# Optimization experiments

Measured on AMD Instinct MI355X. Metric: run time of the kernel, lower is better.

The kernel has to match this reference:

```python
import jax, jax.numpy as jnp
import numpy as np

H1, H2 = 32, 16


def _gru_layer(x, W_ih, W_hh, b_ih, b_hh, H):
    # x: [B, T, I]; W_ih: [3H, I]; W_hh: [3H, H]; biases: [3H]
    # PyTorch gate order: r, z, n
    B = x.shape[0]
    xW = jnp.einsum('bti,gi->btg', x, W_ih) + b_ih  # [B, T, 3H]

    def step(h, xw_t):
        gh = h @ W_hh.T + b_hh                      # [B, 3H]
        r = jax.nn.sigmoid(xw_t[:, :H] + gh[:, :H])
        z = jax.nn.sigmoid(xw_t[:, H:2 * H] + gh[:, H:2 * H])
        n = jnp.tanh(xw_t[:, 2 * H:] + r * gh[:, 2 * H:])
        h_new = (1.0 - z) * n + z * h
        return h_new, h_new

    h0 = jnp.zeros((B, H), dtype=x.dtype)
    _, ys = jax.lax.scan(step, h0, jnp.swapaxes(xW, 0, 1))  # ys: [T, B, H]
    return jnp.swapaxes(ys, 0, 1)


def setup_inputs() -> dict:
    key = jax.random.key(0)
    ks = jax.random.split(key, 11)
    B, I, T, O = 4096, 8, 512, 1

    def u(k, shape, fan):
        s = 1.0 / np.sqrt(fan)
        return jax.random.uniform(k, shape, jnp.float32, -s, s)

    return {
        'input_seq': jax.random.normal(ks[0], (B, I, T), jnp.float32),
        'W_ih1': u(ks[1], (3 * H1, I), H1),
        'W_hh1': u(ks[2], (3 * H1, H1), H1),
        'b_ih1': u(ks[3], (3 * H1,), H1),
        'b_hh1': u(ks[4], (3 * H1,), H1),
        'W_ih2': u(ks[5], (3 * H2, H1), H2),
        'W_hh2': u(ks[6], (3 * H2, H2), H2),
        'b_ih2': u(ks[7], (3 * H2,), H2),
        'b_hh2': u(ks[8], (3 * H2,), H2),
        'W_lin': u(ks[9], (O, H2), H2),
        'b_lin': u(ks[10], (O,), H2),
    }


def reference(input_seq, W_ih1, W_hh1, b_ih1, b_hh1,
              W_ih2, W_hh2, b_ih2, b_hh2, W_lin, b_lin):
    x = jnp.transpose(input_seq, (0, 2, 1))          # [B, T, I]
    h1 = _gru_layer(x, W_ih1, W_hh1, b_ih1, b_hh1, H1)   # [B, T, 32]
    h2 = _gru_layer(h1, W_ih2, W_hh2, b_ih2, b_hh2, H2)  # [B, T, 16]
    out = h2[:, -1, :] @ W_lin.T + b_lin             # [B, O]
    return jnp.squeeze(out)                          # [B] when O == 1
```

## Files before the change

### kernel.cpp

```cpp
#include <hip/hip_runtime.h>

typedef __attribute__((ext_vector_type(4))) float    f32x4;
typedef __attribute__((ext_vector_type(4))) unsigned u32x4;

#define LOG2E 1.44269504088896340736f
__device__ __forceinline__ float fexp2(float x){ return __builtin_amdgcn_exp2f(x); }
__device__ __forceinline__ float frcp (float x){ return __builtin_amdgcn_rcpf(x); }
__device__ __forceinline__ float sigf (float x){ return frcp(1.0f + fexp2(-LOG2E*x)); }
__device__ __forceinline__ float tanh_(float x){ return 1.0f - 2.0f*frcp(1.0f + fexp2(2.0f*LOG2E*x)); }

__device__ __forceinline__ unsigned rne_bf16(float f){
    unsigned u = __builtin_bit_cast(unsigned, f);
    return (u + 0x7fffu + ((u >> 16) & 1u)) >> 16;
}
__device__ __forceinline__ u32x4 packdup4(const float* p){
    u32x4 r;
    #pragma unroll
    for (int q = 0; q < 4; ++q) {
        unsigned w = rne_bf16(p[q]);
        r[q] = w | (w << 16);
    }
    return r;
}
__device__ __forceinline__ unsigned packsplit(float h){
    unsigned hu = __builtin_bit_cast(unsigned, h);
    unsigned hm = hu & 0xffff0000u;
    float rem = h - __builtin_bit_cast(float, hm);
    unsigned ru = __builtin_bit_cast(unsigned, rem);
    return (hm >> 16) | (ru & 0xffff0000u);
}

#define MFMA_INIT(d, a, b, c) asm("v_mfma_f32_16x16x32_bf16 %0, %1, %2, %3" : "=&v"(d) : "v"(a), "v"(b), "v"(c))
#define MFMA_ACC(acc, a, b)   asm("v_mfma_f32_16x16x32_bf16 %0, %1, %2, %0" : "+v"(acc) : "v"(a), "v"(b))

__global__ __launch_bounds__(192)
void gru2_mfma(const float* __restrict__ x_g,
               const float* __restrict__ Wih1, const float* __restrict__ Whh1,
               const float* __restrict__ bih1, const float* __restrict__ bhh1,
               const float* __restrict__ Wih2, const float* __restrict__ Whh2,
               const float* __restrict__ bih2, const float* __restrict__ bhh2,
               const float* __restrict__ Wlin, const float* __restrict__ blin,
               float* __restrict__ out)
{
    const int tid = threadIdx.x;
    const int wid = tid / 64;
    const int l   = tid & 63;
    const int sl  = l & 15;
    const int g   = l >> 4;
    const int b0  = blockIdx.x * 16;

    __shared__ unsigned xpk[32][16][12];
    __shared__ unsigned h1b[2][16][36];
    __shared__ unsigned h2b[2][16][20];
    __shared__ unsigned zl[4];

    {
        unsigned* p1 = &h1b[0][0][0];
        for (int k = tid; k < 2*16*36; k += 192) p1[k] = 0u;
        unsigned* p2 = &h2b[0][0][0];
        for (int k = tid; k < 2*16*20; k += 192) p2[k] = 0u;
        if (tid < 4) zl[tid] = 0u;
    }

    u32x4 fR0, fR1, fR2, fZ0, fZ1, fZ2, fX0, fA, fB;
    f32x4 cbR, cbZ, cbX, cbH;
    const u32x4 zero4 = {0u, 0u, 0u, 0u};

    if (wid < 2) {
        const int Ub = wid * 16;
        const int gr = Ub + sl, gz = 32 + Ub + sl, gn = 64 + Ub + sl;
        fR0 = (g < 2) ? packdup4(Wih1 + gr*8  + 4*g) : zero4;
        fR1 = packdup4(Whh1 + gr*32 + 4*g);
        fR2 = packdup4(Whh1 + gr*32 + 16 + 4*g);
        fZ0 = (g < 2) ? packdup4(Wih1 + gz*8  + 4*g) : zero4;
        fZ1 = packdup4(Whh1 + gz*32 + 4*g);
        fZ2 = packdup4(Whh1 + gz*32 + 16 + 4*g);
        fX0 = (g < 2) ? packdup4(Wih1 + gn*8  + 4*g) : zero4;
        fA  = packdup4(Whh1 + gn*32 + 4*g);
        fB  = packdup4(Whh1 + gn*32 + 16 + 4*g);
        #pragma unroll
        for (int e = 0; e < 4; ++e) {
            const int u = Ub + 4*g + e;
            cbR[e] = bih1[u]      + bhh1[u];
            cbZ[e] = bih1[32+u]   + bhh1[32+u];
            cbX[e] = bih1[64+u];
            cbH[e] = bhh1[64+u];
        }
    } else {
        fR0 = packdup4(Wih2 + sl*32 + 4*g);
        fR1 = packdup4(Wih2 + sl*32 + 16 + 4*g);
        fR2 = packdup4(Whh2 + sl*16 + 4*g);
        fZ0 = packdup4(Wih2 + (16+sl)*32 + 4*g);
        fZ1 = packdup4(Wih2 + (16+sl)*32 + 16 + 4*g);
        fZ2 = packdup4(Whh2 + (16+sl)*16 + 4*g);
        fX0 = packdup4(Wih2 + (32+sl)*32 + 4*g);
        fA  = packdup4(Wih2 + (32+sl)*32 + 16 + 4*g);
        fB  = packdup4(Whh2 + (32+sl)*16 + 4*g);
        #pragma unroll
        for (int e = 0; e < 4; ++e) {
            const int u = 4*g + e;
            cbR[e] = bih2[u]    + bhh2[u];
            cbZ[e] = bih2[16+u] + bhh2[16+u];
            cbX[e] = bih2[32+u];
            cbH[e] = bhh2[32+u];
        }
    }

    float hv[4] = {0.f, 0.f, 0.f, 0.f};

    #pragma unroll 1
    for (int i = 0; i <= 512; ++i) {
        if ((i & 31) == 0 && i < 512) {
            if (tid < 128) {
                const int s  = tid >> 3;
                const int ii = tid & 7;
                const float* xg = x_g + ((size_t)(b0 + s))*4096 + ii*512 + i;
                #pragma unroll
                for (int w4 = 0; w4 < 8; ++w4) {
                    const f32x4 v = *(const f32x4*)(xg + 4*w4);
                    #pragma unroll
                    for (int e = 0; e < 4; ++e)
                        xpk[w4*4 + e][s][ii] = packsplit(v[e]);
                }
            }
            __syncthreads();
        }

        const int pr = (i + 1) & 1;

        if (wid < 2 && i < 512) {
            const int tt = i & 31;
            const u32x4 bT0 = (g < 2) ? *(const u32x4*)&xpk[tt][sl][4*g]
                                      : *(const u32x4*)&zl[0];
            const u32x4 bT1 = *(const u32x4*)&h1b[pr][sl][4*g];
            const u32x4 bT2 = *(const u32x4*)&h1b[pr][sl][16 + 4*g];
            f32x4 cr, cz, cx, cn;
            MFMA_INIT(cr, fR0, bT0, cbR); MFMA_ACC(cr, fR1, bT1); MFMA_ACC(cr, fR2, bT2);
            MFMA_INIT(cz, fZ0, bT0, cbZ); MFMA_ACC(cz, fZ1, bT1); MFMA_ACC(cz, fZ2, bT2);
            MFMA_INIT(cx, fX0, bT0, cbX);
            MFMA_INIT(cn, fA,  bT1, cbH); MFMA_ACC(cn, fB, bT2);
            unsigned wr0, wr1, wr2, wr3;
            {
                float r, z, n, h;
                r = sigf(cr[0]); z = sigf(cz[0]); n = tanh_(fmaf(r, cn[0], cx[0]));
                h = n + z*(hv[0]-n); hv[0] = h; wr0 = packsplit(h);
                r = sigf(cr[1]); z = sigf(cz[1]); n = tanh_(fmaf(r, cn[1], cx[1]));
                h = n + z*(hv[1]-n); hv[1] = h; wr1 = packsplit(h);
                r = sigf(cr[2]); z = sigf(cz[2]); n = tanh_(fmaf(r, cn[2], cx[2]));
                h = n + z*(hv[2]-n); hv[2] = h; wr2 = packsplit(h);
                r = sigf(cr[3]); z = sigf(cz[3]); n = tanh_(fmaf(r, cn[3], cx[3]));
                h = n + z*(hv[3]-n); hv[3] = h; wr3 = packsplit(h);
            }
            u32x4 wv = {wr0, wr1, wr2, wr3};
            *(u32x4*)&h1b[i & 1][sl][(wid ? 16 : 0) + 4*g] = wv;
        }

        if (wid == 2 && i > 0) {
            const u32x4 bU0 = *(const u32x4*)&h1b[pr][sl][4*g];
            const u32x4 bU1 = *(const u32x4*)&h1b[pr][sl][16 + 4*g];
            const u32x4 bU2 = *(const u32x4*)&h2b[i & 1][sl][4*g];
            f32x4 cr, cz, cx, cn;
            MFMA_INIT(cr, fR0, bU0, cbR); MFMA_ACC(cr, fR1, bU1); MFMA_ACC(cr, fR2, bU2);
            MFMA_INIT(cz, fZ0, bU0, cbZ); MFMA_ACC(cz, fZ1, bU1); MFMA_ACC(cz, fZ2, bU2);
            MFMA_INIT(cx, fX0, bU0, cbX); MFMA_ACC(cx, fA, bU1);
            MFMA_INIT(cn, fB,  bU2, cbH);
            unsigned wr0, wr1, wr2, wr3;
            {
                float r, z, n, h;
                r = sigf(cr[0]); z = sigf(cz[0]); n = tanh_(fmaf(r, cn[0], cx[0]));
                h = n + z*(hv[0]-n); hv[0] = h; wr0 = packsplit(h);
                r = sigf(cr[1]); z = sigf(cz[1]); n = tanh_(fmaf(r, cn[1], cx[1]));
                h = n + z*(hv[1]-n); hv[1] = h; wr1 = packsplit(h);
                r = sigf(cr[2]); z = sigf(cz[2]); n = tanh_(fmaf(r, cn[2], cx[2]));
                h = n + z*(hv[2]-n); hv[2] = h; wr2 = packsplit(h);
                r = sigf(cr[3]); z = sigf(cz[3]); n = tanh_(fmaf(r, cn[3], cx[3]));
                h = n + z*(hv[3]-n); hv[3] = h; wr3 = packsplit(h);
            }
            u32x4 wv = {wr0, wr1, wr2, wr3};
            *(u32x4*)&h2b[(i + 1) & 1][sl][4*g] = wv;
        }

        __syncthreads();
    }

    if (wid == 2) {
        float acc = 0.0f;
        acc = fmaf(Wlin[4*g+0], hv[0], acc);
        acc = fmaf(Wlin[4*g+1], hv[1], acc);
        acc = fmaf(Wlin[4*g+2], hv[2], acc);
        acc = fmaf(Wlin[4*g+3], hv[3], acc);
        acc += __shfl_xor(acc, 16, 64);
        acc += __shfl_xor(acc, 32, 64);
        if (g == 0) out[b0 + sl] = acc + blin[0];
    }
}

extern "C" void kernel_launch(void* const* d_in, const int* in_sizes, int n_in,
                              void* d_out, int out_size, void* d_ws, size_t ws_size,
                              hipStream_t stream) {
    const float* x    = (const float*)d_in[0];
    const float* Wih1 = (const float*)d_in[1];
    const float* Whh1 = (const float*)d_in[2];
    const float* bih1 = (const float*)d_in[3];
    const float* bhh1 = (const float*)d_in[4];
    const float* Wih2 = (const float*)d_in[5];
    const float* Whh2 = (const float*)d_in[6];
    const float* bih2 = (const float*)d_in[7];
    const float* bhh2 = (const float*)d_in[8];
    const float* Wlin = (const float*)d_in[9];
    const float* blin = (const float*)d_in[10];
    float* out = (float*)d_out;

    dim3 grid(256), block(192);
    hipLaunchKernelGGL(gru2_mfma, grid, block, 0, stream,
                       x, Wih1, Whh1, bih1, bhh1, Wih2, Whh2, bih2, bhh2,
                       Wlin, blin, out);
}
```

Baseline: 260.2 us.

## Add bf16 low-part weight MFMAs and keep own hidden state in registers

```diff
diff --git a/kernel.cpp b/kernel.cpp
--- a/kernel.cpp
+++ b/kernel.cpp
@@ -2,12 +2,18 @@
 
 typedef __attribute__((ext_vector_type(4))) float    f32x4;
 typedef __attribute__((ext_vector_type(4))) unsigned u32x4;
+typedef __attribute__((ext_vector_type(8))) short    s16x8;
 
 #define LOG2E 1.44269504088896340736f
 __device__ __forceinline__ float fexp2(float x){ return __builtin_amdgcn_exp2f(x); }
 __device__ __forceinline__ float frcp (float x){ return __builtin_amdgcn_rcpf(x); }
 __device__ __forceinline__ float sigf (float x){ return frcp(1.0f + fexp2(-LOG2E*x)); }
 __device__ __forceinline__ float tanh_(float x){ return 1.0f - 2.0f*frcp(1.0f + fexp2(2.0f*LOG2E*x)); }
+
+__device__ __forceinline__ f32x4 mfma16(u32x4 a, u32x4 b, f32x4 c){
+    return __builtin_amdgcn_mfma_f32_16x16x32_bf16(
+        __builtin_bit_cast(s16x8, a), __builtin_bit_cast(s16x8, b), c, 0, 0, 0);
+}
 
 __device__ __forceinline__ unsigned rne_bf16(float f){
     unsigned u = __builtin_bit_cast(unsigned, f);
@@ -22,6 +28,17 @@
     }
     return r;
 }
+__device__ __forceinline__ u32x4 packdup4_lo(const float* p){
+    u32x4 r;
+    #pragma unroll
+    for (int q = 0; q < 4; ++q) {
+        unsigned wh = rne_bf16(p[q]);
+        float    wf = __builtin_bit_cast(float, wh << 16);
+        unsigned wl = rne_bf16(p[q] - wf);
+        r[q] = wl | (wl << 16);
+    }
+    return r;
+}
 __device__ __forceinline__ unsigned packsplit(float h){
     unsigned hu = __builtin_bit_cast(unsigned, h);
     unsigned hm = hu & 0xffff0000u;
@@ -29,9 +46,6 @@
     unsigned ru = __builtin_bit_cast(unsigned, rem);
     return (hm >> 16) | (ru & 0xffff0000u);
 }
-
-#define MFMA_INIT(d, a, b, c) asm("v_mfma_f32_16x16x32_bf16 %0, %1, %2, %3" : "=&v"(d) : "v"(a), "v"(b), "v"(c))
-#define MFMA_ACC(acc, a, b)   asm("v_mfma_f32_16x16x32_bf16 %0, %1, %2, %0" : "+v"(acc) : "v"(a), "v"(b))
 
 __global__ __launch_bounds__(192)
 void gru2_mfma(const float* __restrict__ x_g,
@@ -51,33 +65,40 @@
 
     __shared__ unsigned xpk[32][16][12];
     __shared__ unsigned h1b[2][16][36];
-    __shared__ unsigned h2b[2][16][20];
     __shared__ unsigned zl[4];
 
     {
         unsigned* p1 = &h1b[0][0][0];
         for (int k = tid; k < 2*16*36; k += 192) p1[k] = 0u;
-        unsigned* p2 = &h2b[0][0][0];
-        for (int k = tid; k < 2*16*20; k += 192) p2[k] = 0u;
         if (tid < 4) zl[tid] = 0u;
     }
 
-    u32x4 fR0, fR1, fR2, fZ0, fZ1, fZ2, fX0, fA, fB;
+    u32x4 fR0,fR0l, fR1,fR1l, fR2,fR2l, fZ0,fZ0l, fZ1,fZ1l, fZ2,fZ2l,
+          fX0,fX0l, fA,fAl, fB,fBl;
     f32x4 cbR, cbZ, cbX, cbH;
-    const u32x4 zero4 = {0u, 0u, 0u, 0u};
+    const u32x4 zero4 = {0u,0u,0u,0u};
 
     if (wid < 2) {
         const int Ub = wid * 16;
         const int gr = Ub + sl, gz = 32 + Ub + sl, gn = 64 + Ub + sl;
-        fR0 = (g < 2) ? packdup4(Wih1 + gr*8  + 4*g) : zero4;
-        fR1 = packdup4(Whh1 + gr*32 + 4*g);
-        fR2 = packdup4(Whh1 + gr*32 + 16 + 4*g);
-        fZ0 = (g < 2) ? packdup4(Wih1 + gz*8  + 4*g) : zero4;
-        fZ1 = packdup4(Whh1 + gz*32 + 4*g);
-        fZ2 = packdup4(Whh1 + gz*32 + 16 + 4*g);
-        fX0 = (g < 2) ? packdup4(Wih1 + gn*8  + 4*g) : zero4;
-        fA  = packdup4(Whh1 + gn*32 + 4*g);
-        fB  = packdup4(Whh1 + gn*32 + 16 + 4*g);
+        fR0  = (g < 2) ? packdup4   (Wih1 + gr*8 + 4*g) : zero4;
+        fR0l = (g < 2) ? packdup4_lo(Wih1 + gr*8 + 4*g) : zero4;
+        fR1  = packdup4   (Whh1 + gr*32 + 4*g);
+        fR1l = packdup4_lo(Whh1 + gr*32 + 4*g);
+        fR2  = packdup4   (Whh1 + gr*32 + 16 + 4*g);
+        fR2l = packdup4_lo(Whh1 + gr*32 + 16 + 4*g);
+        fZ0  = (g < 2) ? packdup4   (Wih1 + gz*8 + 4*g) : zero4;
+        fZ0l = (g < 2) ? packdup4_lo(Wih1 + gz*8 + 4*g) : zero4;
+        fZ1  = packdup4   (Whh1 + gz*32 + 4*g);
+        fZ1l = packdup4_lo(Whh1 + gz*32 + 4*g);
+        fZ2  = packdup4   (Whh1 + gz*32 + 16 + 4*g);
+        fZ2l = packdup4_lo(Whh1 + gz*32 + 16 + 4*g);
+        fX0  = (g < 2) ? packdup4   (Wih1 + gn*8 + 4*g) : zero4;
+        fX0l = (g < 2) ? packdup4_lo(Wih1 + gn*8 + 4*g) : zero4;
+        fA   = packdup4   (Whh1 + gn*32 + 4*g);
+        fAl  = packdup4_lo(Whh1 + gn*32 + 4*g);
+        fB   = packdup4   (Whh1 + gn*32 + 16 + 4*g);
+        fBl  = packdup4_lo(Whh1 + gn*32 + 16 + 4*g);
         #pragma unroll
         for (int e = 0; e < 4; ++e) {
             const int u = Ub + 4*g + e;
@@ -87,15 +108,24 @@
             cbH[e] = bhh1[64+u];
         }
     } else {
-        fR0 = packdup4(Wih2 + sl*32 + 4*g);
-        fR1 = packdup4(Wih2 + sl*32 + 16 + 4*g);
-        fR2 = packdup4(Whh2 + sl*16 + 4*g);
-        fZ0 = packdup4(Wih2 + (16+sl)*32 + 4*g);
-        fZ1 = packdup4(Wih2 + (16+sl)*32 + 16 + 4*g);
-        fZ2 = packdup4(Whh2 + (16+sl)*16 + 4*g);
-        fX0 = packdup4(Wih2 + (32+sl)*32 + 4*g);
-        fA  = packdup4(Wih2 + (32+sl)*32 + 16 + 4*g);
-        fB  = packdup4(Whh2 + (32+sl)*16 + 4*g);
+        fR0  = packdup4   (Wih2 + sl*32 + 4*g);
+        fR0l = packdup4_lo(Wih2 + sl*32 + 4*g);
+        fR1  = packdup4   (Wih2 + sl*32 + 16 + 4*g);
+        fR1l = packdup4_lo(Wih2 + sl*32 + 16 + 4*g);
+        fR2  = packdup4   (Whh2 + sl*16 + 4*g);
+        fR2l = packdup4_lo(Whh2 + sl*16 + 4*g);
+        fZ0  = packdup4   (Wih2 + (16+sl)*32 + 4*g);
+        fZ0l = packdup4_lo(Wih2 + (16+sl)*32 + 4*g);
+        fZ1  = packdup4   (Wih2 + (16+sl)*32 + 16 + 4*g);
+        fZ1l = packdup4_lo(Wih2 + (16+sl)*32 + 16 + 4*g);
+        fZ2  = packdup4   (Whh2 + (16+sl)*16 + 4*g);
+        fZ2l = packdup4_lo(Whh2 + (16+sl)*16 + 4*g);
+        fX0  = packdup4   (Wih2 + (32+sl)*32 + 4*g);
+        fX0l = packdup4_lo(Wih2 + (32+sl)*32 + 4*g);
+        fA   = packdup4   (Wih2 + (32+sl)*32 + 16 + 4*g);
+        fAl  = packdup4_lo(Wih2 + (32+sl)*32 + 16 + 4*g);
+        fB   = packdup4   (Whh2 + (32+sl)*16 + 4*g);
+        fBl  = packdup4_lo(Whh2 + (32+sl)*16 + 4*g);
         #pragma unroll
         for (int e = 0; e < 4; ++e) {
             const int u = 4*g + e;
@@ -106,7 +136,9 @@
         }
     }
 
-    float hv[4] = {0.f, 0.f, 0.f, 0.f};
+    float hv[4] = {0.f,0.f,0.f,0.f};
+    u32x4 own   = {0u,0u,0u,0u};
+    const f32x4 zc = {0.f,0.f,0.f,0.f};
 
     #pragma unroll 1
     for (int i = 0; i <= 512; ++i) {
@@ -132,52 +164,52 @@
             const int tt = i & 31;
             const u32x4 bT0 = (g < 2) ? *(const u32x4*)&xpk[tt][sl][4*g]
                                       : *(const u32x4*)&zl[0];
-            const u32x4 bT1 = *(const u32x4*)&h1b[pr][sl][4*g];
-            const u32x4 bT2 = *(const u32x4*)&h1b[pr][sl][16 + 4*g];
-            f32x4 cr, cz, cx, cn;
-            MFMA_INIT(cr, fR0, bT0, cbR); MFMA_ACC(cr, fR1, bT1); MFMA_ACC(cr, fR2, bT2);
-            MFMA_INIT(cz, fZ0, bT0, cbZ); MFMA_ACC(cz, fZ1, bT1); MFMA_ACC(cz, fZ2, bT2);
-            MFMA_INIT(cx, fX0, bT0, cbX);
-            MFMA_INIT(cn, fA,  bT1, cbH); MFMA_ACC(cn, fB, bT2);
-            unsigned wr0, wr1, wr2, wr3;
-            {
-                float r, z, n, h;
-                r = sigf(cr[0]); z = sigf(cz[0]); n = tanh_(fmaf(r, cn[0], cx[0]));
-                h = n + z*(hv[0]-n); hv[0] = h; wr0 = packsplit(h);
-                r = sigf(cr[1]); z = sigf(cz[1]); n = tanh_(fmaf(r, cn[1], cx[1]));
-                h = n + z*(hv[1]-n); hv[1] = h; wr1 = packsplit(h);
-                r = sigf(cr[2]); z = sigf(cz[2]); n = tanh_(fmaf(r, cn[2], cx[2]));
-                h = n + z*(hv[2]-n); hv[2] = h; wr2 = packsplit(h);
-                r = sigf(cr[3]); z = sigf(cz[3]); n = tanh_(fmaf(r, cn[3], cx[3]));
-                h = n + z*(hv[3]-n); hv[3] = h; wr3 = packsplit(h);
+            u32x4 bT1, bT2;
+            if (wid == 0) { bT1 = own;
+                            bT2 = *(const u32x4*)&h1b[pr][sl][16 + 4*g]; }
+            else          { bT1 = *(const u32x4*)&h1b[pr][sl][4*g];
+                            bT2 = own; }
+            f32x4 crh, crl, czh, czl, cx, cnh, cnl;
+            crh = mfma16(fR0,  bT0, cbR); crh = mfma16(fR1,  bT1, crh); crh = mfma16(fR2,  bT2, crh);
+            crl = mfma16(fR0l, bT0, zc ); crl = mfma16(fR1l, bT1, crl); crl = mfma16(fR2l, bT2, crl);
+            czh = mfma16(fZ0,  bT0, cbZ); czh = mfma16(fZ1,  bT1, czh); czh = mfma16(fZ2,  bT2, czh);
+            czl = mfma16(fZ0l, bT0, zc ); czl = mfma16(fZ1l, bT1, czl); czl = mfma16(fZ2l, bT2, czl);
+            cx  = mfma16(fX0,  bT0, cbX); cx  = mfma16(fX0l, bT0, cx );
+            cnh = mfma16(fA,   bT1, cbH); cnh = mfma16(fB,   bT2, cnh);
+            cnl = mfma16(fAl,  bT1, zc ); cnl = mfma16(fBl,  bT2, cnl);
+            #pragma unroll
+            for (int e = 0; e < 4; ++e) {
+                const float r = sigf(crh[e] + crl[e]);
+                const float z = sigf(czh[e] + czl[e]);
+                const float n = tanh_(fmaf(r, cnh[e] + cnl[e], cx[e]));
+                const float h = n + z*(hv[e] - n);
+                hv[e] = h;
+                own[e] = packsplit(h);
             }
-            u32x4 wv = {wr0, wr1, wr2, wr3};
-            *(u32x4*)&h1b[i & 1][sl][(wid ? 16 : 0) + 4*g] = wv;
+            *(u32x4*)&h1b[i & 1][sl][(wid ? 16 : 0) + 4*g] = own;
         }
 
         if (wid == 2 && i > 0) {
             const u32x4 bU0 = *(const u32x4*)&h1b[pr][sl][4*g];
             const u32x4 bU1 = *(const u32x4*)&h1b[pr][sl][16 + 4*g];
-            const u32x4 bU2 = *(const u32x4*)&h2b[i & 1][sl][4*g];
-            f32x4 cr, cz, cx, cn;
-            MFMA_INIT(cr, fR0, bU0, cbR); MFMA_ACC(cr, fR1, bU1); MFMA_ACC(cr, fR2, bU2);
-            MFMA_INIT(cz, fZ0, bU0, cbZ); MFMA_ACC(cz, fZ1, bU1); MFMA_ACC(cz, fZ2, bU2);
-            MFMA_INIT(cx, fX0, bU0, cbX); MFMA_ACC(cx, fA, bU1);
-            MFMA_INIT(cn, fB,  bU2, cbH);
-            unsigned wr0, wr1, wr2, wr3;
-            {
-                float r, z, n, h;
-                r = sigf(cr[0]); z = sigf(cz[0]); n = tanh_(fmaf(r, cn[0], cx[0]));
-                h = n + z*(hv[0]-n); hv[0] = h; wr0 = packsplit(h);
-                r = sigf(cr[1]); z = sigf(cz[1]); n = tanh_(fmaf(r, cn[1], cx[1]));
-                h = n + z*(hv[1]-n); hv[1] = h; wr1 = packsplit(h);
-                r = sigf(cr[2]); z = sigf(cz[2]); n = tanh_(fmaf(r, cn[2], cx[2]));
-                h = n + z*(hv[2]-n); hv[2] = h; wr2 = packsplit(h);
-                r = sigf(cr[3]); z = sigf(cz[3]); n = tanh_(fmaf(r, cn[3], cx[3]));
-                h = n + z*(hv[3]-n); hv[3] = h; wr3 = packsplit(h);
+            const u32x4 bU2 = own;
+            f32x4 crh, crl, czh, czl, cx, cn;
+            crh = mfma16(fR0,  bU0, cbR); crh = mfma16(fR1,  bU1, crh); crh = mfma16(fR2,  bU2, crh);
+            crl = mfma16(fR0l, bU0, zc ); crl = mfma16(fR1l, bU1, crl); crl = mfma16(fR2l, bU2, crl);
+            czh = mfma16(fZ0,  bU0, cbZ); czh = mfma16(fZ1,  bU1, czh); czh = mfma16(fZ2,  bU2, czh);
+            czl = mfma16(fZ0l, bU0, zc ); czl = mfma16(fZ1l, bU1, czl); czl = mfma16(fZ2l, bU2, czl);
+            cx  = mfma16(fX0,  bU0, cbX); cx  = mfma16(fA,   bU1, cx );
+            cx  = mfma16(fX0l, bU0, cx ); cx  = mfma16(fAl,  bU1, cx );
+            cn  = mfma16(fB,   bU2, cbH); cn  = mfma16(fBl,  bU2, cn );
+            #pragma unroll
+            for (int e = 0; e < 4; ++e) {
+                const float r = sigf(crh[e] + crl[e]);
+                const float z = sigf(czh[e] + czl[e]);
+                const float n = tanh_(fmaf(r, cn[e], cx[e]));
+                const float h = n + z*(hv[e] - n);
+                hv[e] = h;
+                own[e] = packsplit(h);
             }
-            u32x4 wv = {wr0, wr1, wr2, wr3};
-            *(u32x4*)&h2b[(i + 1) & 1][sl][4*g] = wv;
         }
 
         __syncthreads();
```

New measurement: 311.6 us. 19.8% more time.
